# Performance work log

Hardware: AMD Instinct MI355X
Metric: run time of the kernel (lower is better)

## Reference

```python
import jax, jax.numpy as jnp
import numpy as np

N = 10000
E = 320000
D = 256   # hidden_dim
H = 4     # heads
C = D // H
NL = 3    # gat layers
EPS = 1e-5


def _ln(x, g, b):
    m = x.mean(-1, keepdims=True)
    v = ((x - m) ** 2).mean(-1, keepdims=True)
    return (x - m) / jnp.sqrt(v + EPS) * g + b


def setup_inputs() -> dict:
    key = jax.random.key(0)
    ks = iter(jax.random.split(key, 64))
    rn = lambda shape, s=0.05: jax.random.normal(next(ks), shape, dtype=jnp.float32) * s
    inp = dict(
        x=jax.random.normal(next(ks), (N, 10), dtype=jnp.float32),
        edge_index=jax.random.randint(next(ks), (2, E), 0, N),
        edge_attr=jax.random.uniform(next(ks), (E, 3), dtype=jnp.float32),
        agent_features=jax.random.normal(next(ks), (1, 10), dtype=jnp.float32),
        # node encoder
        enc_w=rn((10, D)), enc_b=jnp.zeros(D), enc_g=jnp.ones(D), enc_bt=jnp.zeros(D),
        # adaptive virtual node
        vn_base=jnp.zeros(D), vn_w1=rn((D, D)), vn_b1=jnp.zeros(D),
        vn_g=jnp.ones(D), vn_bt=jnp.zeros(D), vn_w2=rn((D, D)), vn_b2=jnp.zeros(D),
        # stacked GAT layer params
        gat_w=rn((NL, D, D)), att_src=rn((NL, H, C)), att_dst=rn((NL, H, C)),
        att_edge=rn((NL, H, C)), edge_w=rn((NL, 3, D)), gat_b=jnp.zeros((NL, D)),
        ln_g=jnp.ones((NL, D)), ln_b=jnp.zeros((NL, D)),
        # agent encoder
        ag_w=rn((10, D)), ag_b=jnp.zeros(D), ag_g=jnp.ones(D), ag_bt=jnp.zeros(D),
        # dueling heads (jk_dim = D*(NL+1) + D)
        v_w1=rn((D * (NL + 2), D)), v_b1=jnp.zeros(D), v_g=jnp.ones(D), v_bt=jnp.zeros(D),
        v_w2=rn((D, 1)), v_b2=jnp.zeros(1),
        a_w1=rn((D * (NL + 2), D)), a_b1=jnp.zeros(D), a_g=jnp.ones(D), a_bt=jnp.zeros(D),
        a_w2=rn((D, 9)), a_b2=jnp.zeros(9),
    )
    return inp


def _gat_layer(h, src, dst, eattr, lin_w, a_s, a_d, a_e, e_w, bias, n_seg):
    xs = (h @ lin_w).reshape(-1, H, C)                       # [Nt,H,C]
    al_s = (xs * a_s).sum(-1)                                # [Nt,H]
    al_d = (xs * a_d).sum(-1)
    ee = (eattr @ e_w).reshape(-1, H, C)                     # [Et,H,C]
    al_e = (ee * a_e).sum(-1)                                # [Et,H]
    alpha = jax.nn.leaky_relu(al_s[src] + al_d[dst] + al_e, 0.2)
    mx = jax.ops.segment_max(alpha, dst, num_segments=n_seg)
    a = jnp.exp(alpha - mx[dst])
    s = jax.ops.segment_sum(a, dst, num_segments=n_seg)
    a = a / (s[dst] + 1e-16)
    msg = xs[src] * a[:, :, None]                            # [Et,H,C]
    out = jax.ops.segment_sum(msg, dst, num_segments=n_seg)
    return out.reshape(n_seg, D) + bias


def reference(x, edge_index, edge_attr, agent_features,
              enc_w, enc_b, enc_g, enc_bt,
              vn_base, vn_w1, vn_b1, vn_g, vn_bt, vn_w2, vn_b2,
              gat_w, att_src, att_dst, att_edge, edge_w, gat_b, ln_g, ln_b,
              ag_w, ag_b, ag_g, ag_bt,
              v_w1, v_b1, v_g, v_bt, v_w2, v_b2,
              a_w1, a_b1, a_g, a_bt, a_w2, a_b2):
    n = x.shape[0]
    nt = n + 1  # + virtual node
    h0 = jax.nn.relu(_ln(x @ enc_w + enc_b, enc_g, enc_bt))
    ctx = h0.mean(0)
    ad = jnp.tanh(jax.nn.relu(_ln(ctx @ vn_w1 + vn_b1, vn_g, vn_bt)) @ vn_w2 + vn_b2)
    vn = vn_base + ad
    h = jnp.concatenate([h0, vn[None]], axis=0)              # [Nt,D]

    # virtual-node edges (bidirectional) with edge_attr = [0.5,0,0]
    ar = jnp.arange(n)
    vfull = jnp.full((n,), n, dtype=edge_index.dtype)
    src0 = jnp.concatenate([edge_index[0], vfull, ar])
    dst0 = jnp.concatenate([edge_index[1], ar, vfull])
    veattr = jnp.concatenate([jnp.full((2 * n, 1), 0.5), jnp.zeros((2 * n, 2))], axis=1)
    eattr0 = jnp.concatenate([edge_attr, veattr], axis=0)

    # GATConv add_self_loops with fill_value='mean' (mean of incoming edge_attr)
    deg = jax.ops.segment_sum(jnp.ones_like(dst0, dtype=jnp.float32), dst0, num_segments=nt)
    loop_attr = jax.ops.segment_sum(eattr0, dst0, num_segments=nt) / jnp.maximum(deg, 1.0)[:, None]
    loops = jnp.arange(nt, dtype=edge_index.dtype)
    src = jnp.concatenate([src0, loops])
    dst = jnp.concatenate([dst0, loops])
    eattr = jnp.concatenate([eattr0, loop_attr], axis=0)

    outs = [h]
    for i in range(NL):
        hn = _gat_layer(h, src, dst, eattr, gat_w[i], att_src[i], att_dst[i],
                        att_edge[i], edge_w[i], gat_b[i], nt)
        hn = _ln(hn, ln_g[i], ln_b[i])
        h = jax.nn.relu(hn + h)
        outs.append(h)
    jk = jnp.concatenate(outs, axis=-1)                      # [Nt, D*(NL+1)]

    global_repr = jk[-1][None]                               # virtual node row
    agent = jax.nn.relu(_ln(agent_features @ ag_w + ag_b, ag_g, ag_bt))
    comb = jnp.concatenate([global_repr, agent], axis=-1)
    val = jax.nn.relu(_ln(comb @ v_w1 + v_b1, v_g, v_bt)) @ v_w2 + v_b2
    adv = jax.nn.relu(_ln(comb @ a_w1 + a_b1, a_g, a_bt)) @ a_w2 + a_b2
    return val + (adv - adv.mean(axis=1, keepdims=True))
```

## Files before the change

### kernel.cpp

```cpp
#include <hip/hip_runtime.h>
#include <math.h>

#define NN 10000
#define EE 320000
#define DD 256
#define NT 10001
#define E1C (EE + NN)
#define E2C (EE + 2 * NN)
#define ETC (E2C + NT)
#define VB 157

typedef __attribute__((ext_vector_type(8))) short s16x8;
typedef __attribute__((ext_vector_type(4))) float f32x4;

__device__ __forceinline__ unsigned short f2bf(float f) {
    unsigned u = __float_as_uint(f);
    return (unsigned short)((u + 0x7FFFu + ((u >> 16) & 1u)) >> 16);
}
__device__ __forceinline__ float bf2f(unsigned short u) {
    return __uint_as_float((unsigned)u << 16);
}

__device__ __forceinline__ float wave_sum(float v) {
#pragma unroll
    for (int o = 32; o > 0; o >>= 1) v += __shfl_down(v, o, 64);
    return v;
}
__device__ __forceinline__ float blk_sum256(float v, float* sm4) {
    v = wave_sum(v);
    int lane = threadIdx.x & 63, w = threadIdx.x >> 6;
    __syncthreads();
    if (lane == 0) sm4[w] = v;
    __syncthreads();
    return sm4[0] + sm4[1] + sm4[2] + sm4[3];
}
__device__ __forceinline__ float2 blk_sum2(float a, float b, float2* sm4) {
#pragma unroll
    for (int o = 32; o > 0; o >>= 1) {
        a += __shfl_down(a, o, 64);
        b += __shfl_down(b, o, 64);
    }
    int lane = threadIdx.x & 63, w = threadIdx.x >> 6;
    __syncthreads();
    if (lane == 0) sm4[w] = make_float2(a, b);
    __syncthreads();
    float2 r;
    r.x = sm4[0].x + sm4[1].x + sm4[2].x + sm4[3].x;
    r.y = sm4[0].y + sm4[1].y + sm4[2].y + sm4[3].y;
    return r;
}

__global__ void __launch_bounds__(256) k_enc(
        const float* __restrict__ x, const float* __restrict__ wenc,
        const float* __restrict__ bia, const float* __restrict__ g,
        const float* __restrict__ bt, float* __restrict__ h,
        unsigned short* __restrict__ hb) {
    int t = threadIdx.x, lane = t & 63, wv = t >> 6;
    int v = blockIdx.x * 4 + wv;
    if (v >= NN) return;
    float xv = (lane < 10) ? x[v * 10 + lane] : 0.f;
    float4 acc = *(const float4*)(bia + lane * 4);
#pragma unroll
    for (int k = 0; k < 10; k++) {
        float xk = __shfl(xv, k, 64);
        float4 wk = *(const float4*)(wenc + k * DD + lane * 4);
        acc.x += xk * wk.x; acc.y += xk * wk.y; acc.z += xk * wk.z; acc.w += xk * wk.w;
    }
    float s1 = acc.x + acc.y + acc.z + acc.w;
    float s2 = acc.x * acc.x + acc.y * acc.y + acc.z * acc.z + acc.w * acc.w;
#pragma unroll
    for (int o = 32; o > 0; o >>= 1) {
        s1 += __shfl_xor(s1, o, 64);
        s2 += __shfl_xor(s2, o, 64);
    }
    float m = s1 * (1.f / DD);
    float var = s2 * (1.f / DD) - m * m;
    float rs = rsqrtf(var + 1e-5f);
    float4 g4 = *(const float4*)(g + lane * 4);
    float4 b4 = *(const float4*)(bt + lane * 4);
    float4 r4;
    r4.x = fmaxf((acc.x - m) * rs * g4.x + b4.x, 0.f);
    r4.y = fmaxf((acc.y - m) * rs * g4.y + b4.y, 0.f);
    r4.z = fmaxf((acc.z - m) * rs * g4.z + b4.z, 0.f);
    r4.w = fmaxf((acc.w - m) * rs * g4.w + b4.w, 0.f);
    *(float4*)(h + (size_t)v * DD + lane * 4) = r4;
    ushort4 u4;
    u4.x = f2bf(r4.x); u4.y = f2bf(r4.y); u4.z = f2bf(r4.z); u4.w = f2bf(r4.w);
    *(ushort4*)(hb + (size_t)v * DD + lane * 4) = u4;
}

__global__ void __launch_bounds__(256) k_ctx1deg(const float* __restrict__ h,
                                                 float* __restrict__ part,
                                                 const int* __restrict__ ei,
                                                 int* __restrict__ degi) {
    __shared__ float4 sm[4][64];
    int t = threadIdx.x, lane = t & 63, w = t >> 6;
    int b = blockIdx.x;
    float4 acc = make_float4(0.f, 0.f, 0.f, 0.f);
    for (int v = b * 4 + w; v < NN; v += 1024) {
        float4 hv = *(const float4*)(h + (size_t)v * DD + lane * 4);
        acc.x += hv.x; acc.y += hv.y; acc.z += hv.z; acc.w += hv.w;
    }
    sm[w][lane] = acc;
    __syncthreads();
    if (t < 64) {
        float4 a0 = sm[0][t], a1 = sm[1][t], a2 = sm[2][t], a3 = sm[3][t];
        float4 r;
        r.x = a0.x + a1.x + a2.x + a3.x;
        r.y = a0.y + a1.y + a2.y + a3.y;
        r.z = a0.z + a1.z + a2.z + a3.z;
        r.w = a0.w + a1.w + a2.w + a3.w;
        *(float4*)(part + (size_t)b * DD + t * 4) = r;
    }
    for (int e = b * 256 + t; e < EE; e += 256 * 256)
        atomicAdd(&degi[ei[EE + e]], 1);
}

__global__ void k_vn(const float* __restrict__ part,
                     const float* __restrict__ w1, const float* __restrict__ b1,
                     const float* __restrict__ g, const float* __restrict__ bt,
                     const float* __restrict__ w2, const float* __restrict__ b2,
                     const float* __restrict__ vnb,
                     float* __restrict__ h, unsigned short* __restrict__ hb,
                     float* __restrict__ comb) {
    __shared__ float2 sm4[4];
    __shared__ float cs[DD];
    __shared__ float t[DD];
    int j = threadIdx.x;
    float c = 0.f;
    for (int b = 0; b < 256; b++) c += part[(size_t)b * DD + j];
    cs[j] = c * (1.f / NN);
    __syncthreads();
    float acc = b1[j];
    for (int k = 0; k < DD; k++) acc += cs[k] * w1[k * DD + j];
    float2 mm = blk_sum2(acc, acc * acc, sm4);
    float m = mm.x * (1.f / DD);
    float var = mm.y * (1.f / DD) - m * m;
    float y = fmaxf((acc - m) * rsqrtf(var + 1e-5f) * g[j] + bt[j], 0.f);
    t[j] = y;
    __syncthreads();
    float a2 = b2[j];
    for (int k = 0; k < DD; k++) a2 += t[k] * w2[k * DD + j];
    float vn = vnb[j] + tanhf(a2);
    h[(size_t)NN * DD + j] = vn;
    hb[(size_t)NN * DD + j] = f2bf(vn);
    comb[j] = vn;
}

__global__ void k_scan(const int* __restrict__ degi, int* __restrict__ offs,
                       int* __restrict__ cursor) {
    __shared__ int wsum[16];
    __shared__ int running_s;
    int t = threadIdx.x, lane = t & 63, w = t >> 6;
    if (t == 0) running_s = 0;
    __syncthreads();
    for (int base = 0; base < NT; base += 1024) {
        int v = base + t;
        int val = 0;
        if (v < NN) val = degi[v] + 2;
        else if (v == NN) val = NN + 1;
        int x = val;
#pragma unroll
        for (int o = 1; o < 64; o <<= 1) {
            int y = __shfl_up(x, o, 64);
            if (lane >= o) x += y;
        }
        if (lane == 63) wsum[w] = x;
        __syncthreads();
        int prefix = running_s;
        for (int ww = 0; ww < w; ww++) prefix += wsum[ww];
        if (v <= NN) { int e0 = prefix + x - val; offs[v] = e0; cursor[v] = e0; }
        __syncthreads();
        if (t == 0) {
            int s = 0;
            for (int i = 0; i < 16; i++) s += wsum[i];
            running_s += s;
        }
        __syncthreads();
    }
    if (threadIdx.x == 0) offs[NT] = running_s;
}

__global__ void k_scatter(const int* __restrict__ ei, int* __restrict__ cursor,
                          int* __restrict__ ssrc, int* __restrict__ seid) {
    int e = blockIdx.x * 256 + threadIdx.x;
    if (e >= EE) return;
    int src = ei[e], dst = ei[EE + e];
    int pos = atomicAdd(&cursor[dst], 1);
    ssrc[pos] = src;
    seid[pos] = e;
}

__global__ void k_flattr(const int* __restrict__ offs, int* __restrict__ ssrc,
                         int* __restrict__ seid,
                         const float* __restrict__ ea, float* __restrict__ lattr) {
    int t = threadIdx.x, lane = t & 63, w = t >> 6;
    int v = blockIdx.x * 4 + w;
    if (v > NN) return;
    int bN = offs[NN];
    if (v == NN) {
        if (lane == 0) {
            lattr[v * 3] = 0.5f; lattr[v * 3 + 1] = 0.f; lattr[v * 3 + 2] = 0.f;
            ssrc[bN + NN] = NN; seid[bN + NN] = E2C + NN;
        }
        return;
    }
    int b0 = offs[v], e1 = offs[v + 1];
    if (lane == 0) {
        ssrc[e1 - 2] = NN; seid[e1 - 2] = EE + v;
        ssrc[e1 - 1] = v;  seid[e1 - 1] = E2C + v;
        ssrc[bN + v] = v;  seid[bN + v] = E1C + v;
    }
    int cnt = e1 - b0 - 2;
    float s0 = 0.f, s1 = 0.f, s2 = 0.f;
    for (int i = lane; i < cnt; i += 64) {
        int e = seid[b0 + i];
        s0 += ea[e * 3];
        s1 += ea[e * 3 + 1];
        s2 += ea[e * 3 + 2];
    }
    s0 = wave_sum(s0); s1 = wave_sum(s1); s2 = wave_sum(s2);
    if (lane == 0) {
        float inv = 1.f / (float)(cnt + 1);
        lattr[v * 3]     = (s0 + 0.5f) * inv;
        lattr[v * 3 + 1] = s1 * inv;
        lattr[v * 3 + 2] = s2 * inv;
    }
}

__global__ void k_wconv(const float* __restrict__ gw, unsigned short* __restrict__ wt,
                        const float* __restrict__ ew, const float* __restrict__ ae,
                        float* __restrict__ wd) {
    int b = blockIdx.x, j = threadIdx.x;
    if (b == 768) {
        if (j >= 36) return;
        int l = j / 12, k = (j / 4) % 3, h = j % 4;
        float s = 0.f;
        for (int c = 0; c < 64; c++)
            s += ew[l * 768 + k * DD + h * 64 + c] * ae[l * DD + h * 64 + c];
        wd[j] = s;
        return;
    }
    int l = b >> 8, k = b & 255;
    float v = gw[l * 65536 + k * 256 + j];
    wt[l * 65536 + j * 256 + k] = f2bf(v);
}

__global__ void k_edot(const int* __restrict__ seid, const float* __restrict__ ea,
                       const float* __restrict__ lattr, const float* __restrict__ wd,
                       unsigned short* __restrict__ edot) {
    int p = blockIdx.x * 256 + threadIdx.x;
    if (p >= ETC) return;
    int e = seid[p];
    float a0, a1, a2;
    if (e < EE)       { a0 = ea[e * 3]; a1 = ea[e * 3 + 1]; a2 = ea[e * 3 + 2]; }
    else if (e < E2C) { a0 = 0.5f; a1 = 0.f; a2 = 0.f; }
    else              { int v = e - E2C; a0 = lattr[v * 3]; a1 = lattr[v * 3 + 1]; a2 = lattr[v * 3 + 2]; }
#pragma unroll
    for (int l = 0; l < 3; l++) {
        ushort4 o;
        o.x = f2bf(a0 * wd[l * 12 + 0] + a1 * wd[l * 12 + 4] + a2 * wd[l * 12 + 8]);
        o.y = f2bf(a0 * wd[l * 12 + 1] + a1 * wd[l * 12 + 5] + a2 * wd[l * 12 + 9]);
        o.z = f2bf(a0 * wd[l * 12 + 2] + a1 * wd[l * 12 + 6] + a2 * wd[l * 12 + 10]);
        o.w = f2bf(a0 * wd[l * 12 + 3] + a1 * wd[l * 12 + 7] + a2 * wd[l * 12 + 11]);
        *(ushort4*)(edot + (size_t)l * ETC * 4 + (size_t)p * 4) = o;
    }
}

__global__ void __launch_bounds__(256) k_gemm_mfma(
        const unsigned short* __restrict__ hb, const unsigned short* __restrict__ wt,
        const float* __restrict__ as_, const float* __restrict__ ad_,
        unsigned short* __restrict__ xsb, float* __restrict__ als, float* __restrict__ ald) {
    __shared__ unsigned short tile[64][256];
    int t = threadIdx.x, lane = t & 63, w = t >> 6;
    int v0 = blockIdx.x * 64;
    int rbase = v0 + w * 16;
    int li = lane & 15, g = lane >> 4;
    int arow = rbase + li; if (arow > NN) arow = NN;
    int koff = g * 8;
    const unsigned short* aptr = hb + (size_t)arow * DD + koff;
    const unsigned short* bptr = wt + (size_t)li * DD + koff;
    f32x4 acc[16];
#pragma unroll
    for (int n = 0; n < 16; n++) acc[n] = (f32x4){0.f, 0.f, 0.f, 0.f};
#pragma unroll
    for (int kb = 0; kb < 8; kb++) {
        s16x8 af = *(const s16x8*)(aptr + kb * 32);
#pragma unroll
        for (int n = 0; n < 16; n++) {
            s16x8 bf = *(const s16x8*)(bptr + (size_t)n * 16 * DD + kb * 32);
            acc[n] = __builtin_amdgcn_mfma_f32_16x16x32_bf16(af, bf, acc[n], 0, 0, 0);
        }
    }
    float asv[16], adv[16];
#pragma unroll
    for (int n = 0; n < 16; n++) { asv[n] = as_[n * 16 + li]; adv[n] = ad_[n * 16 + li]; }
#pragma unroll
    for (int r = 0; r < 4; r++) {
        int vrow = rbase + 4 * g + r;
#pragma unroll
        for (int h = 0; h < 4; h++) {
            float ps = acc[4 * h][r] * asv[4 * h] + acc[4 * h + 1][r] * asv[4 * h + 1]
                     + acc[4 * h + 2][r] * asv[4 * h + 2] + acc[4 * h + 3][r] * asv[4 * h + 3];
            float pd = acc[4 * h][r] * adv[4 * h] + acc[4 * h + 1][r] * adv[4 * h + 1]
                     + acc[4 * h + 2][r] * adv[4 * h + 2] + acc[4 * h + 3][r] * adv[4 * h + 3];
#pragma unroll
            for (int o = 1; o < 16; o <<= 1) {
                ps += __shfl_xor(ps, o, 64);
                pd += __shfl_xor(pd, o, 64);
            }
            if (li == 0 && vrow <= NN) { als[vrow * 4 + h] = ps; ald[vrow * 4 + h] = pd; }
        }
    }
#pragma unroll
    for (int n = 0; n < 16; n++)
#pragma unroll
        for (int r = 0; r < 4; r++)
            tile[w * 16 + 4 * g + r][n * 16 + li] = f2bf(acc[n][r]);
#pragma unroll
    for (int it = 0; it < 8; it++) {
        int flat = it * 64 + lane;
        int row = w * 16 + (flat >> 5);
        int c8 = flat & 31;
        int vrow = v0 + row;
        if (vrow <= NN)
            *(uint4*)(xsb + (size_t)vrow * DD + c8 * 8) = *(const uint4*)(&tile[row][c8 * 8]);
    }
}

__global__ void __launch_bounds__(256) k_msg(
        const int* __restrict__ offs, const int* __restrict__ ssrc,
        const unsigned short* __restrict__ edotL,
        const float* __restrict__ als, const float* __restrict__ ald,
        const unsigned short* __restrict__ xsb,
        const float* __restrict__ bias, const float* __restrict__ g,
        const float* __restrict__ bt, const float* __restrict__ hin,
        float* __restrict__ hout, unsigned short* __restrict__ hbout,
        float* __restrict__ pvacc, float* __restrict__ pws) {
    int v = blockIdx.x;
    if (v == NN) return;
    int t = threadIdx.x, lane = t & 63, w = t >> 6;
    int sub = lane >> 5, l32 = lane & 31, slot = w * 2 + sub;
    int hh = l32 >> 3;
    __shared__ float red[4][8][33];
    __shared__ float wsred[4][4];
    __shared__ float fin[4];
    __shared__ float2 sm4[4];
    float acc[8];
#pragma unroll
    for (int q = 0; q < 8; q++) acc[q] = 0.f;
    float swt = 0.f;
    if (v >= NT) {
        int b = v - NT;
        int b0 = offs[NN];
        float adh = ald[NN * 4 + hh];
        int i0 = b * 64, i1 = i0 + 64;
        if (i1 > NN + 1) i1 = NN + 1;
        for (int i = i0 + slot; i < i1; i += 8) {
            float a = als[i * 4 + hh] + bf2f(edotL[(size_t)(b0 + i) * 4 + hh]) + adh;
            a = a > 0.f ? a : 0.2f * a;
            float wt = __expf(a);
            uint4 xq = *(const uint4*)(xsb + (size_t)i * DD + l32 * 8);
            const unsigned short* xp = (const unsigned short*)&xq;
#pragma unroll
            for (int q = 0; q < 8; q++) acc[q] += wt * bf2f(xp[q]);
            if ((l32 & 7) == 0) swt += wt;
        }
#pragma unroll
        for (int q = 0; q < 8; q++) acc[q] += __shfl_xor(acc[q], 32, 64);
        swt += __shfl_xor(swt, 32, 64);
        if (sub == 0) {
#pragma unroll
            for (int q = 0; q < 8; q++) red[w][q][l32] = acc[q];
            if ((l32 & 7) == 0) wsred[w][hh] = swt;
        }
        __syncthreads();
        int c = t, q = c & 7, l = c >> 3;
        pvacc[(size_t)b * DD + c] = red[0][q][l] + red[1][q][l] + red[2][q][l] + red[3][q][l];
        if (t < 4) pws[b * 4 + t] = wsred[0][t] + wsred[1][t] + wsred[2][t] + wsred[3][t];
        return;
    }
    int b0 = offs[v], deg = offs[v + 1] - b0;
    float adh = ald[v * 4 + hh];
    for (int i = slot; i < deg; i += 8) {
        int p = b0 + i;
        int src = ssrc[p];
        float a = als[src * 4 + hh] + bf2f(edotL[(size_t)p * 4 + hh]) + adh;
        a = a > 0.f ? a : 0.2f * a;
        float wt = __expf(a);
        uint4 xq = *(const uint4*)(xsb + (size_t)src * DD + l32 * 8);
        const unsigned short* xp = (const unsigned short*)&xq;
#pragma unroll
        for (int q = 0; q < 8; q++) acc[q] += wt * bf2f(xp[q]);
        if ((l32 & 7) == 0) swt += wt;
    }
#pragma unroll
    for (int q = 0; q < 8; q++) acc[q] += __shfl_xor(acc[q], 32, 64);
    swt += __shfl_xor(swt, 32, 64);
    if (sub == 0) {
#pragma unroll
        for (int q = 0; q < 8; q++) red[w][q][l32] = acc[q];
        if ((l32 & 7) == 0) wsred[w][hh] = swt;
    }
    __syncthreads();
    if (t < 4) {
        float ws = wsred[0][t] + wsred[1][t] + wsred[2][t] + wsred[3][t];
        fin[t] = 1.f / (ws + 1e-16f);
    }
    __syncthreads();
    int c = t, q = c & 7, l = c >> 3;
    float o = (red[0][q][l] + red[1][q][l] + red[2][q][l] + red[3][q][l]) * fin[c >> 6];
    float tt = o + bias[c];
    float2 mm = blk_sum2(tt, tt * tt, sm4);
    float m = mm.x * (1.f / DD);
    float var = mm.y * (1.f / DD) - m * m;
    float y = (tt - m) * rsqrtf(var + 1e-5f) * g[c] + bt[c];
    float r = fmaxf(y + hin[(size_t)v * DD + c], 0.f);
    hout[(size_t)v * DD + c] = r;
    hbout[(size_t)v * DD + c] = f2bf(r);
}

__global__ void k_vpost(const float* __restrict__ pvacc, const float* __restrict__ pws,
                        const float* __restrict__ bias, const float* __restrict__ g,
                        const float* __restrict__ bt, const float* __restrict__ hin,
                        float* __restrict__ hout, unsigned short* __restrict__ hb,
                        float* __restrict__ jkslot,
                        int last, const float* __restrict__ af,
                        const float* __restrict__ agw, const float* __restrict__ agb,
                        const float* __restrict__ agg, const float* __restrict__ agbt,
                        float* __restrict__ comb) {
    __shared__ float2 sm4[4];
    int j = threadIdx.x, hh = j >> 6;
    float acc = 0.f;
    for (int b = 0; b < VB; b++) acc += pvacc[(size_t)b * DD + j];
    float ws = 0.f;
    for (int b = 0; b < VB; b++) ws += pws[b * 4 + hh];
    float o = acc / (ws + 1e-16f);
    float tt = o + bias[j];
    float2 mm = blk_sum2(tt, tt * tt, sm4);
    float m = mm.x * (1.f / DD);
    float var = mm.y * (1.f / DD) - m * m;
    float y = (tt - m) * rsqrtf(var + 1e-5f) * g[j] + bt[j];
    float r = fmaxf(y + hin[(size_t)NN * DD + j], 0.f);
    hout[(size_t)NN * DD + j] = r;
    hb[(size_t)NN * DD + j] = f2bf(r);
    jkslot[j] = r;
    if (last) {
        float a2 = agb[j];
#pragma unroll
        for (int k = 0; k < 10; k++) a2 += af[k] * agw[k * DD + j];
        float2 m2 = blk_sum2(a2, a2 * a2, sm4);
        float mu = m2.x * (1.f / DD);
        float vv = m2.y * (1.f / DD) - mu * mu;
        float ya = (a2 - mu) * rsqrtf(vv + 1e-5f) * agg[j] + agbt[j];
        comb[1024 + j] = fmaxf(ya, 0.f);
    }
}

__global__ void k_head1(const float* __restrict__ comb,
                        const float* __restrict__ vw1, const float* __restrict__ aw1,
                        float* __restrict__ pv, float* __restrict__ pa) {
    int j = threadIdx.x, s = blockIdx.x;
    int k0 = s * 32;
    float accv = 0.f, acca = 0.f;
#pragma unroll
    for (int kk = 0; kk < 32; kk++) {
        float c = comb[k0 + kk];
        accv += c * vw1[(k0 + kk) * DD + j];
        acca += c * aw1[(k0 + kk) * DD + j];
    }
    pv[s * DD + j] = accv;
    pa[s * DD + j] = acca;
}

__global__ void k_head2(const float* __restrict__ pv, const float* __restrict__ pa,
                        const float* __restrict__ vb1, const float* __restrict__ vg,
                        const float* __restrict__ vbt, const float* __restrict__ vw2,
                        const float* __restrict__ vb2,
                        const float* __restrict__ ab1, const float* __restrict__ ag,
                        const float* __restrict__ abt, const float* __restrict__ aw2,
                        const float* __restrict__ ab2, float* __restrict__ out) {
    __shared__ float2 sm4[4];
    __shared__ float sm1[4];
    __shared__ float tl[DD];
    __shared__ float adv[9];
    __shared__ float valv;
    int j = threadIdx.x;
    float acc = vb1[j], acc2 = ab1[j];
    for (int s = 0; s < 40; s++) { acc += pv[s * DD + j]; acc2 += pa[s * DD + j]; }
    float2 mm = blk_sum2(acc, acc * acc, sm4);
    float m = mm.x * (1.f / DD);
    float var = mm.y * (1.f / DD) - m * m;
    float y = fmaxf((acc - m) * rsqrtf(var + 1e-5f) * vg[j] + vbt[j], 0.f);
    float vs = blk_sum256(y * vw2[j], sm1);
    if (j == 0) valv = vs + vb2[0];
    float2 mm2 = blk_sum2(acc2, acc2 * acc2, sm4);
    float m2 = mm2.x * (1.f / DD);
    float var2 = mm2.y * (1.f / DD) - m2 * m2;
    float y2 = fmaxf((acc2 - m2) * rsqrtf(var2 + 1e-5f) * ag[j] + abt[j], 0.f);
    tl[j] = y2;
    __syncthreads();
    if (j < 9) {
        float s = ab2[j];
        for (int k = 0; k < DD; k++) s += tl[k] * aw2[k * 9 + j];
        adv[j] = s;
    }
    __syncthreads();
    if (j < 9) {
        float mean = 0.f;
        for (int o = 0; o < 9; o++) mean += adv[o];
        mean *= (1.f / 9.f);
        out[j] = valv + adv[j] - mean;
    }
}

extern "C" void kernel_launch(void* const* d_in, const int* in_sizes, int n_in,
                              void* d_out, int out_size, void* d_ws, size_t ws_size,
                              hipStream_t stream) {
    (void)in_sizes; (void)n_in; (void)out_size; (void)ws_size;
    const float* x      = (const float*)d_in[0];
    const int*   ei     = (const int*)d_in[1];
    const float* ea     = (const float*)d_in[2];
    const float* af     = (const float*)d_in[3];
    const float* enc_w  = (const float*)d_in[4];
    const float* enc_b  = (const float*)d_in[5];
    const float* enc_g  = (const float*)d_in[6];
    const float* enc_bt = (const float*)d_in[7];
    const float* vn_base= (const float*)d_in[8];
    const float* vn_w1  = (const float*)d_in[9];
    const float* vn_b1  = (const float*)d_in[10];
    const float* vn_g   = (const float*)d_in[11];
    const float* vn_bt  = (const float*)d_in[12];
    const float* vn_w2  = (const float*)d_in[13];
    const float* vn_b2  = (const float*)d_in[14];
    const float* gat_w  = (const float*)d_in[15];
    const float* att_src= (const float*)d_in[16];
    const float* att_dst= (const float*)d_in[17];
    const float* att_edge=(const float*)d_in[18];
    const float* edge_w = (const float*)d_in[19];
    const float* gat_b  = (const float*)d_in[20];
    const float* ln_g   = (const float*)d_in[21];
    const float* ln_b   = (const float*)d_in[22];
    const float* ag_w   = (const float*)d_in[23];
    const float* ag_b   = (const float*)d_in[24];
    const float* ag_g   = (const float*)d_in[25];
    const float* ag_bt  = (const float*)d_in[26];
    const float* v_w1   = (const float*)d_in[27];
    const float* v_b1   = (const float*)d_in[28];
    const float* v_g    = (const float*)d_in[29];
    const float* v_bt   = (const float*)d_in[30];
    const float* v_w2   = (const float*)d_in[31];
    const float* v_b2   = (const float*)d_in[32];
    const float* a_w1   = (const float*)d_in[33];
    const float* a_b1   = (const float*)d_in[34];
    const float* a_g    = (const float*)d_in[35];
    const float* a_bt   = (const float*)d_in[36];
    const float* a_w2   = (const float*)d_in[37];
    const float* a_b2   = (const float*)d_in[38];

    char* p = (char*)d_ws;
    auto alloc = [&](size_t bytes) {
        char* r = p;
        p += (bytes + 255) & ~(size_t)255;
        return r;
    };
    float* big0  = (float*)alloc((size_t)NT * DD * 4);
    float* big2  = (float*)alloc((size_t)NT * DD * 4);
    unsigned short* hb   = (unsigned short*)alloc((size_t)NT * DD * 2);
    unsigned short* xsb  = (unsigned short*)alloc((size_t)NT * DD * 2);
    unsigned short* wt   = (unsigned short*)alloc((size_t)3 * DD * DD * 2);
    unsigned short* edot = (unsigned short*)alloc((size_t)3 * ETC * 4 * 2);
    int* ssrc    = (int*)alloc((size_t)ETC * 4);
    int* seid    = (int*)alloc((size_t)ETC * 4);
    float* als   = (float*)alloc((size_t)NT * 4 * 4);
    float* ald   = (float*)alloc((size_t)NT * 4 * 4);
    float* part  = (float*)alloc((size_t)256 * DD * 4);
    float* comb  = (float*)alloc(1280 * 4);
    float* lattr = (float*)alloc((size_t)NT * 3 * 4);
    float* wd    = (float*)alloc(36 * 4);
    float* pvacc = (float*)alloc((size_t)VB * DD * 4);
    float* pws   = (float*)alloc((size_t)VB * 4 * 4);
    float* pv    = (float*)alloc(40 * DD * 4);
    float* pa    = (float*)alloc(40 * DD * 4);
    int* degi    = (int*)alloc((size_t)NT * 4);
    int* offs    = (int*)alloc((size_t)(NT + 1) * 4);
    int* cursor  = (int*)alloc((size_t)NT * 4);

    hipMemsetAsync(degi, 0, (size_t)NT * 4, stream);

    k_enc<<<2500, 256, 0, stream>>>(x, enc_w, enc_b, enc_g, enc_bt, big0, hb);
    k_ctx1deg<<<256, 256, 0, stream>>>(big0, part, ei, degi);
    k_vn<<<1, 256, 0, stream>>>(part, vn_w1, vn_b1, vn_g, vn_bt, vn_w2, vn_b2, vn_base, big0, hb, comb);
    k_scan<<<1, 1024, 0, stream>>>(degi, offs, cursor);
    k_scatter<<<(EE + 255) / 256, 256, 0, stream>>>(ei, cursor, ssrc, seid);
    k_flattr<<<(NT + 3) / 4, 256, 0, stream>>>(offs, ssrc, seid, ea, lattr);
    k_wconv<<<769, 256, 0, stream>>>(gat_w, wt, edge_w, att_edge, wd);
    k_edot<<<(ETC + 255) / 256, 256, 0, stream>>>(seid, ea, lattr, wd, edot);

    float* cur = big0;
    float* po  = big2;
    for (int l = 0; l < 3; l++) {
        const unsigned short* edotL = edot + (size_t)l * ETC * 4;
        k_gemm_mfma<<<(NT + 63) / 64, 256, 0, stream>>>(hb, wt + (size_t)l * DD * DD,
                                                        att_src + l * DD, att_dst + l * DD,
                                                        xsb, als, ald);
        k_msg<<<NT + VB, 256, 0, stream>>>(offs, ssrc, edotL, als, ald, xsb,
                                           gat_b + l * DD, ln_g + l * DD, ln_b + l * DD,
                                           cur, po, hb, pvacc, pws);
        k_vpost<<<1, 256, 0, stream>>>(pvacc, pws, gat_b + l * DD, ln_g + l * DD, ln_b + l * DD,
                                       cur, po, hb, comb + (l + 1) * DD,
                                       (l == 2) ? 1 : 0, af, ag_w, ag_b, ag_g, ag_bt, comb);
        float* t = cur; cur = po; po = t;
    }
    k_head1<<<40, 256, 0, stream>>>(comb, v_w1, a_w1, pv, pa);
    k_head2<<<1, 256, 0, stream>>>(pv, pa, v_b1, v_g, v_bt, v_w2, v_b2,
                                   a_b1, a_g, a_bt, a_w2, a_b2, (float*)d_out);
}
```

Baseline: 405.3 us.

## Split GEMM over output halves and fuse tail reductions via last-block atomics

The MFMA projection GEMM now splits each 64-row tile into two 128-column halves, doubling the block count and halving accumulator registers so more blocks run at once on the GPU. The separate virtual-node post-processing kernel is folded into k_msg: the last virtual-node block, detected through an atomic counter with threadfences, performs the final reduction and LayerNorm. The two dueling-head kernels are merged the same way. This removes four launches per forward pass, at the cost of atomic counters (zeroed by the existing memset) and serial tail work inside one block.

```diff
diff --git a/kernel.cpp b/kernel.cpp
--- a/kernel.cpp
+++ b/kernel.cpp
@@ -271,35 +271,38 @@
         const unsigned short* __restrict__ hb, const unsigned short* __restrict__ wt,
         const float* __restrict__ as_, const float* __restrict__ ad_,
         unsigned short* __restrict__ xsb, float* __restrict__ als, float* __restrict__ ald) {
-    __shared__ unsigned short tile[64][256];
+    __shared__ unsigned short tile[64][128];
+    int bx = blockIdx.x;
+    int v0 = (bx >> 1) * 64;
+    int n0 = (bx & 1) * 128;
     int t = threadIdx.x, lane = t & 63, w = t >> 6;
-    int v0 = blockIdx.x * 64;
     int rbase = v0 + w * 16;
     int li = lane & 15, g = lane >> 4;
     int arow = rbase + li; if (arow > NN) arow = NN;
     int koff = g * 8;
     const unsigned short* aptr = hb + (size_t)arow * DD + koff;
-    const unsigned short* bptr = wt + (size_t)li * DD + koff;
-    f32x4 acc[16];
-#pragma unroll
-    for (int n = 0; n < 16; n++) acc[n] = (f32x4){0.f, 0.f, 0.f, 0.f};
+    const unsigned short* bptr = wt + (size_t)(n0 + li) * DD + koff;
+    f32x4 acc[8];
+#pragma unroll
+    for (int n = 0; n < 8; n++) acc[n] = (f32x4){0.f, 0.f, 0.f, 0.f};
 #pragma unroll
     for (int kb = 0; kb < 8; kb++) {
         s16x8 af = *(const s16x8*)(aptr + kb * 32);
 #pragma unroll
-        for (int n = 0; n < 16; n++) {
+        for (int n = 0; n < 8; n++) {
             s16x8 bf = *(const s16x8*)(bptr + (size_t)n * 16 * DD + kb * 32);
             acc[n] = __builtin_amdgcn_mfma_f32_16x16x32_bf16(af, bf, acc[n], 0, 0, 0);
         }
     }
-    float asv[16], adv[16];
-#pragma unroll
-    for (int n = 0; n < 16; n++) { asv[n] = as_[n * 16 + li]; adv[n] = ad_[n * 16 + li]; }
+    float asv[8], adv[8];
+#pragma unroll
+    for (int n = 0; n < 8; n++) { asv[n] = as_[n0 + n * 16 + li]; adv[n] = ad_[n0 + n * 16 + li]; }
+    int hg0 = n0 >> 6;
 #pragma unroll
     for (int r = 0; r < 4; r++) {
         int vrow = rbase + 4 * g + r;
 #pragma unroll
-        for (int h = 0; h < 4; h++) {
+        for (int h = 0; h < 2; h++) {
             float ps = acc[4 * h][r] * asv[4 * h] + acc[4 * h + 1][r] * asv[4 * h + 1]
                      + acc[4 * h + 2][r] * asv[4 * h + 2] + acc[4 * h + 3][r] * asv[4 * h + 3];
             float pd = acc[4 * h][r] * adv[4 * h] + acc[4 * h + 1][r] * adv[4 * h + 1]
@@ -309,22 +312,22 @@
                 ps += __shfl_xor(ps, o, 64);
                 pd += __shfl_xor(pd, o, 64);
             }
-            if (li == 0 && vrow <= NN) { als[vrow * 4 + h] = ps; ald[vrow * 4 + h] = pd; }
-        }
-    }
-#pragma unroll
-    for (int n = 0; n < 16; n++)
+            if (li == 0 && vrow <= NN) { als[vrow * 4 + hg0 + h] = ps; ald[vrow * 4 + hg0 + h] = pd; }
+        }
+    }
+#pragma unroll
+    for (int n = 0; n < 8; n++)
 #pragma unroll
         for (int r = 0; r < 4; r++)
             tile[w * 16 + 4 * g + r][n * 16 + li] = f2bf(acc[n][r]);
 #pragma unroll
-    for (int it = 0; it < 8; it++) {
+    for (int it = 0; it < 4; it++) {
         int flat = it * 64 + lane;
-        int row = w * 16 + (flat >> 5);
-        int c8 = flat & 31;
+        int row = w * 16 + (flat >> 4);
+        int c8 = flat & 15;
         int vrow = v0 + row;
         if (vrow <= NN)
-            *(uint4*)(xsb + (size_t)vrow * DD + c8 * 8) = *(const uint4*)(&tile[row][c8 * 8]);
+            *(uint4*)(xsb + (size_t)vrow * DD + n0 + c8 * 8) = *(const uint4*)(&tile[row][c8 * 8]);
     }
 }
 
@@ -336,7 +339,12 @@
         const float* __restrict__ bias, const float* __restrict__ g,
         const float* __restrict__ bt, const float* __restrict__ hin,
         float* __restrict__ hout, unsigned short* __restrict__ hbout,
-        float* __restrict__ pvacc, float* __restrict__ pws) {
+        float* __restrict__ pvacc, float* __restrict__ pws,
+        int* __restrict__ cnt, float* __restrict__ jkslot,
+        int last, const float* __restrict__ af,
+        const float* __restrict__ agw, const float* __restrict__ agb,
+        const float* __restrict__ agg, const float* __restrict__ agbt,
+        float* __restrict__ comb) {
     int v = blockIdx.x;
     if (v == NN) return;
     int t = threadIdx.x, lane = t & 63, w = t >> 6;
@@ -346,6 +354,7 @@
     __shared__ float wsred[4][4];
     __shared__ float fin[4];
     __shared__ float2 sm4[4];
+    __shared__ int islast;
     float acc[8];
 #pragma unroll
     for (int q = 0; q < 8; q++) acc[q] = 0.f;
@@ -378,6 +387,36 @@
         int c = t, q = c & 7, l = c >> 3;
         pvacc[(size_t)b * DD + c] = red[0][q][l] + red[1][q][l] + red[2][q][l] + red[3][q][l];
         if (t < 4) pws[b * 4 + t] = wsred[0][t] + wsred[1][t] + wsred[2][t] + wsred[3][t];
+        __threadfence();
+        if (t == 0) islast = (atomicAdd(cnt, 1) == VB - 1) ? 1 : 0;
+        __syncthreads();
+        if (!islast) return;
+        __threadfence();
+        int j = t, hh4 = j >> 6;
+        float va = 0.f;
+        for (int bb = 0; bb < VB; bb++) va += pvacc[(size_t)bb * DD + j];
+        float ws = 0.f;
+        for (int bb = 0; bb < VB; bb++) ws += pws[bb * 4 + hh4];
+        float o = va / (ws + 1e-16f);
+        float tt = o + bias[j];
+        float2 mm = blk_sum2(tt, tt * tt, sm4);
+        float m = mm.x * (1.f / DD);
+        float var = mm.y * (1.f / DD) - m * m;
+        float y = (tt - m) * rsqrtf(var + 1e-5f) * g[j] + bt[j];
+        float r = fmaxf(y + hin[(size_t)NN * DD + j], 0.f);
+        hout[(size_t)NN * DD + j] = r;
+        hbout[(size_t)NN * DD + j] = f2bf(r);
+        jkslot[j] = r;
+        if (last) {
+            float a2 = agb[j];
+#pragma unroll
+            for (int k = 0; k < 10; k++) a2 += af[k] * agw[k * DD + j];
+            float2 m2 = blk_sum2(a2, a2 * a2, sm4);
+            float mu = m2.x * (1.f / DD);
+            float vv = m2.y * (1.f / DD) - mu * mu;
+            float ya = (a2 - mu) * rsqrtf(vv + 1e-5f) * agg[j] + agbt[j];
+            comb[1024 + j] = fmaxf(ya, 0.f);
+        }
         return;
     }
     int b0 = offs[v], deg = offs[v + 1] - b0;
@@ -420,74 +459,40 @@
     hbout[(size_t)v * DD + c] = f2bf(r);
 }
 
-__global__ void k_vpost(const float* __restrict__ pvacc, const float* __restrict__ pws,
-                        const float* __restrict__ bias, const float* __restrict__ g,
-                        const float* __restrict__ bt, const float* __restrict__ hin,
-                        float* __restrict__ hout, unsigned short* __restrict__ hb,
-                        float* __restrict__ jkslot,
-                        int last, const float* __restrict__ af,
-                        const float* __restrict__ agw, const float* __restrict__ agb,
-                        const float* __restrict__ agg, const float* __restrict__ agbt,
-                        float* __restrict__ comb) {
-    __shared__ float2 sm4[4];
-    int j = threadIdx.x, hh = j >> 6;
-    float acc = 0.f;
-    for (int b = 0; b < VB; b++) acc += pvacc[(size_t)b * DD + j];
-    float ws = 0.f;
-    for (int b = 0; b < VB; b++) ws += pws[b * 4 + hh];
-    float o = acc / (ws + 1e-16f);
-    float tt = o + bias[j];
-    float2 mm = blk_sum2(tt, tt * tt, sm4);
-    float m = mm.x * (1.f / DD);
-    float var = mm.y * (1.f / DD) - m * m;
-    float y = (tt - m) * rsqrtf(var + 1e-5f) * g[j] + bt[j];
-    float r = fmaxf(y + hin[(size_t)NN * DD + j], 0.f);
-    hout[(size_t)NN * DD + j] = r;
-    hb[(size_t)NN * DD + j] = f2bf(r);
-    jkslot[j] = r;
-    if (last) {
-        float a2 = agb[j];
-#pragma unroll
-        for (int k = 0; k < 10; k++) a2 += af[k] * agw[k * DD + j];
-        float2 m2 = blk_sum2(a2, a2 * a2, sm4);
-        float mu = m2.x * (1.f / DD);
-        float vv = m2.y * (1.f / DD) - mu * mu;
-        float ya = (a2 - mu) * rsqrtf(vv + 1e-5f) * agg[j] + agbt[j];
-        comb[1024 + j] = fmaxf(ya, 0.f);
-    }
-}
-
-__global__ void k_head1(const float* __restrict__ comb,
-                        const float* __restrict__ vw1, const float* __restrict__ aw1,
-                        float* __restrict__ pv, float* __restrict__ pa) {
-    int j = threadIdx.x, s = blockIdx.x;
-    int k0 = s * 32;
-    float accv = 0.f, acca = 0.f;
-#pragma unroll
-    for (int kk = 0; kk < 32; kk++) {
-        float c = comb[k0 + kk];
-        accv += c * vw1[(k0 + kk) * DD + j];
-        acca += c * aw1[(k0 + kk) * DD + j];
-    }
-    pv[s * DD + j] = accv;
-    pa[s * DD + j] = acca;
-}
-
-__global__ void k_head2(const float* __restrict__ pv, const float* __restrict__ pa,
-                        const float* __restrict__ vb1, const float* __restrict__ vg,
-                        const float* __restrict__ vbt, const float* __restrict__ vw2,
-                        const float* __restrict__ vb2,
-                        const float* __restrict__ ab1, const float* __restrict__ ag,
-                        const float* __restrict__ abt, const float* __restrict__ aw2,
-                        const float* __restrict__ ab2, float* __restrict__ out) {
+__global__ void k_head(const float* __restrict__ comb,
+                       const float* __restrict__ vw1, const float* __restrict__ aw1,
+                       float* __restrict__ pv, float* __restrict__ pa,
+                       int* __restrict__ cnt,
+                       const float* __restrict__ vb1, const float* __restrict__ vg,
+                       const float* __restrict__ vbt, const float* __restrict__ vw2,
+                       const float* __restrict__ vb2,
+                       const float* __restrict__ ab1, const float* __restrict__ ag,
+                       const float* __restrict__ abt, const float* __restrict__ aw2,
+                       const float* __restrict__ ab2, float* __restrict__ out) {
     __shared__ float2 sm4[4];
     __shared__ float sm1[4];
     __shared__ float tl[DD];
     __shared__ float adv[9];
     __shared__ float valv;
-    int j = threadIdx.x;
+    __shared__ int islast;
+    int j = threadIdx.x, s = blockIdx.x;
+    int k0 = s * 32;
+    float accv = 0.f, acca = 0.f;
+#pragma unroll
+    for (int kk = 0; kk < 32; kk++) {
+        float c = comb[k0 + kk];
+        accv += c * vw1[(k0 + kk) * DD + j];
+        acca += c * aw1[(k0 + kk) * DD + j];
+    }
+    pv[s * DD + j] = accv;
+    pa[s * DD + j] = acca;
+    __threadfence();
+    if (j == 0) islast = (atomicAdd(cnt, 1) == 39) ? 1 : 0;
+    __syncthreads();
+    if (!islast) return;
+    __threadfence();
     float acc = vb1[j], acc2 = ab1[j];
-    for (int s = 0; s < 40; s++) { acc += pv[s * DD + j]; acc2 += pa[s * DD + j]; }
+    for (int ss = 0; ss < 40; ss++) { acc += pv[ss * DD + j]; acc2 += pa[ss * DD + j]; }
     float2 mm = blk_sum2(acc, acc * acc, sm4);
     float m = mm.x * (1.f / DD);
     float var = mm.y * (1.f / DD) - m * m;
@@ -501,9 +506,9 @@
     tl[j] = y2;
     __syncthreads();
     if (j < 9) {
-        float s = ab2[j];
-        for (int k = 0; k < DD; k++) s += tl[k] * aw2[k * 9 + j];
-        adv[j] = s;
+        float ss = ab2[j];
+        for (int k = 0; k < DD; k++) ss += tl[k] * aw2[k * 9 + j];
+        adv[j] = ss;
     }
     __syncthreads();
     if (j < 9) {
@@ -582,11 +587,12 @@
     float* pws   = (float*)alloc((size_t)VB * 4 * 4);
     float* pv    = (float*)alloc(40 * DD * 4);
     float* pa    = (float*)alloc(40 * DD * 4);
-    int* degi    = (int*)alloc((size_t)NT * 4);
+    int* degi    = (int*)alloc((size_t)(NT + 16) * 4);
+    int* cnt     = degi + NT;
     int* offs    = (int*)alloc((size_t)(NT + 1) * 4);
     int* cursor  = (int*)alloc((size_t)NT * 4);
 
-    hipMemsetAsync(degi, 0, (size_t)NT * 4, stream);
+    hipMemsetAsync(degi, 0, (size_t)(NT + 16) * 4, stream);
 
     k_enc<<<2500, 256, 0, stream>>>(x, enc_w, enc_b, enc_g, enc_bt, big0, hb);
     k_ctx1deg<<<256, 256, 0, stream>>>(big0, part, ei, degi);
@@ -601,18 +607,17 @@
     float* po  = big2;
     for (int l = 0; l < 3; l++) {
         const unsigned short* edotL = edot + (size_t)l * ETC * 4;
-        k_gemm_mfma<<<(NT + 63) / 64, 256, 0, stream>>>(hb, wt + (size_t)l * DD * DD,
-                                                        att_src + l * DD, att_dst + l * DD,
-                                                        xsb, als, ald);
+        k_gemm_mfma<<<((NT + 63) / 64) * 2, 256, 0, stream>>>(hb, wt + (size_t)l * DD * DD,
+                                                              att_src + l * DD, att_dst + l * DD,
+                                                              xsb, als, ald);
         k_msg<<<NT + VB, 256, 0, stream>>>(offs, ssrc, edotL, als, ald, xsb,
                                            gat_b + l * DD, ln_g + l * DD, ln_b + l * DD,
-                                           cur, po, hb, pvacc, pws);
-        k_vpost<<<1, 256, 0, stream>>>(pvacc, pws, gat_b + l * DD, ln_g + l * DD, ln_b + l * DD,
-                                       cur, po, hb, comb + (l + 1) * DD,
-                                       (l == 2) ? 1 : 0, af, ag_w, ag_b, ag_g, ag_bt, comb);
+                                           cur, po, hb, pvacc, pws, cnt + l,
+                                           comb + (l + 1) * DD, (l == 2) ? 1 : 0,
+                                           af, ag_w, ag_b, ag_g, ag_bt, comb);
         float* t = cur; cur = po; po = t;
     }
-    k_head1<<<40, 256, 0, stream>>>(comb, v_w1, a_w1, pv, pa);
-    k_head2<<<1, 256, 0, stream>>>(pv, pa, v_b1, v_g, v_bt, v_w2, v_b2,
+    k_head<<<40, 256, 0, stream>>>(comb, v_w1, a_w1, pv, pa, cnt + 3,
+                                   v_b1, v_g, v_bt, v_w2, v_b2,
                                    a_b1, a_g, a_bt, a_w2, a_b2, (float*)d_out);
 }
```

Result: no change. 404.5 us (-0.2%).
